# Kernel tuning notes

Hardware: AMD Instinct MI355X
Metric: run time of the kernel (lower is better)

The kernel has to match this reference:

```python
import jax, jax.numpy as jnp
import numpy as np

D_IN = 784
D_Z = 100
N_SAMP = 10
LOG_2PI = float(np.log(2.0 * np.pi))


def setup_inputs() -> dict:
    key = jax.random.key(0)
    ks = jax.random.split(key, 8)
    B = 16384
    x = jax.random.uniform(ks[0], (B, D_IN), dtype=jnp.float32)
    s = 0.05  # small init scale so softplus/sigmoid stay in a sane range
    W0 = jax.random.normal(ks[1], (D_Z, D_IN), dtype=jnp.float32) * s
    b0 = jax.random.normal(ks[2], (D_Z,), dtype=jnp.float32) * s
    W1 = jax.random.normal(ks[3], (D_Z, D_IN), dtype=jnp.float32) * s
    b1 = jax.random.normal(ks[4], (D_Z,), dtype=jnp.float32) * s
    W2 = jax.random.normal(ks[5], (D_IN, D_Z), dtype=jnp.float32) * s
    b2 = jax.random.normal(ks[6], (D_IN,), dtype=jnp.float32) * s
    eps = jax.random.normal(ks[7], (N_SAMP, D_Z), dtype=jnp.float32)  # pz.sample([10])
    return {"x": x, "W0": W0, "b0": b0, "W1": W1, "b1": b1, "W2": W2, "b2": b2, "eps": eps}


def reference(x, W0, b0, W1, b1, W2, b2, eps):
    # encoder: per-dim mean over the batch of softplus(Linear(x))
    mean = jnp.mean(jax.nn.softplus(x @ W0.T + b0), axis=0)        # [D_Z]
    cov = jnp.mean(jax.nn.softplus(x @ W1.T + b1), axis=0)         # [D_Z] (diag variances)
    # z = mean + covariance * eps, eps ~ N(0, I)
    z = mean + cov * eps                                           # [N_SAMP, D_Z]
    y = z @ W2.T + b2                                              # [N_SAMP, D_IN]
    p = jax.nn.sigmoid((2.0 * x[:, None, :] - 1.0) * y[None, :, :])  # [B, N_SAMP, D_IN]
    pv_z = jnp.prod(p, axis=-1) + 0.001                            # [B, N_SAMP]
    E_px_v = jnp.mean(jnp.log(pv_z))
    # diagonal-Gaussian log probs (equivalent to the MVN with eye*cov)
    log_pz = -0.5 * jnp.sum(z * z, axis=-1) - 0.5 * D_Z * LOG_2PI
    log_q = (-0.5 * jnp.sum((z - mean) ** 2 / cov, axis=-1)
             - 0.5 * jnp.sum(jnp.log(cov)) - 0.5 * D_Z * LOG_2PI)
    Dkl = jnp.mean(log_pz - log_q)
    return -(E_px_v + Dkl)
```

## Files before the change

kernel.cpp:

```cpp
#include <hip/hip_runtime.h>
#include <hip/hip_bf16.h>
#include <math.h>

#define NROWS 16384
#define DIN   784
#define DZ    100
#define NS    10
#define NCT   16
#define KTILES 25
#define BND_THR 45.0f
#define KTPAD 520

typedef unsigned short ushort_t;
typedef short bf16x8 __attribute__((ext_vector_type(8)));
typedef float f32x4  __attribute__((ext_vector_type(4)));

#define WS_Y2 208
#define WB_OFF_BYTES (64u * 1024u)

__device__ __forceinline__ float softplus_fast(float v) {
    float t = v * 1.44269504088896f;
    return (fmaxf(t, 0.f)
            + __builtin_amdgcn_logf(1.f + __builtin_amdgcn_exp2f(-fabsf(t))))
           * 0.69314718055995f;
}
__device__ __forceinline__ unsigned pack2(float lo, float hi) {
    float2 f2; f2.x = lo; f2.y = hi;
    __hip_bfloat162 h2 = __float22bfloat162_rn(f2);
    return *reinterpret_cast<unsigned*>(&h2);
}

__global__ __launch_bounds__(256) void wb_kernel(
    const float* __restrict__ W0, const float* __restrict__ W1,
    ushort_t* __restrict__ Wb, float* __restrict__ ws)
{
    if (blockIdx.x == 0) ws[threadIdx.x] = 0.f;
    int t = blockIdx.x * 256 + threadIdx.x;
    if (t >= KTILES * NCT * 64) return;
    int kt = t >> 10;
    int r  = t & 1023;
    int ct = r >> 6, l = r & 63;
    int col = ct * 16 + (l & 15);
    int k0  = kt * 32 + (l >> 4) * 8;
    uint4 o = make_uint4(0u, 0u, 0u, 0u);
    if (col < 200 && k0 < DIN) {
        const float* src = (col < 100 ? W0 + (size_t)col * DIN
                                      : W1 + (size_t)(col - 100) * DIN) + k0;
        float4 a = *(const float4*)src;
        float4 b = *(const float4*)(src + 4);
        o.x = pack2(a.x, a.y); o.y = pack2(a.z, a.w);
        o.z = pack2(b.x, b.y); o.w = pack2(b.z, b.w);
    }
    *(uint4*)(Wb + (size_t)t * 8) = o;
}

__global__ __launch_bounds__(1024) void colmean_g(
    const float* __restrict__ x, const ushort_t* __restrict__ Wb,
    const float* __restrict__ b0, const float* __restrict__ b1,
    float* __restrict__ ws)
{
    __shared__ ushort_t xls[4 * KTILES * KTPAD];
    __shared__ float red2[12][4][16];
    const int tid = threadIdx.x;
    const int lane = tid & 63, w = tid >> 6;
    const int row0 = blockIdx.x * 64;

    for (int slot = tid; slot < 6400; slot += 1024) {
        int r  = slot / 100;
        int sl = slot - r * 100;
        int kt = sl >> 2, kc = sl & 3;
        int k0 = kt * 32 + kc * 8;
        uint4 o = make_uint4(0u, 0u, 0u, 0u);
        if (k0 + 8 <= DIN) {
            const float* src = x + (size_t)(row0 + r) * DIN + k0;
            float4 a = *(const float4*)src, b = *(const float4*)(src + 4);
            o.x = pack2(a.x, a.y); o.y = pack2(a.z, a.w);
            o.z = pack2(b.x, b.y); o.w = pack2(b.z, b.w);
        }
        int l = (kc << 4) | (r & 15);
        *(uint4*)&xls[((size_t)(r >> 4) * KTILES + kt) * KTPAD + l * 8] = o;
    }
    __syncthreads();

    const int rt = w >> 2, ct0 = (w & 3) * 4;
    const ushort_t* ap  = xls + (size_t)rt * KTILES * KTPAD + lane * 8;
    const ushort_t* wbp = Wb + (size_t)ct0 * 512 + lane * 8;

    f32x4 acc[4];
#pragma unroll
    for (int jj = 0; jj < 4; ++jj) acc[jj] = (f32x4){0.f, 0.f, 0.f, 0.f};

    bf16x8 Aa, Ab;
    uint4  Ba[4], Bb[4];

    auto ld = [&](int kt, bf16x8& A, uint4 (&B)[4]) {
        A = *(const bf16x8*)(ap + (size_t)kt * KTPAD);
#pragma unroll
        for (int jj = 0; jj < 4; ++jj)
            B[jj] = *(const uint4*)(wbp + (size_t)kt * 8192 + jj * 512);
    };
    auto cp = [&](const bf16x8& A, const uint4 (&B)[4]) {
#pragma unroll
        for (int jj = 0; jj < 4; ++jj)
            acc[jj] = __builtin_amdgcn_mfma_f32_16x16x32_bf16(
                A, *(const bf16x8*)&B[jj], acc[jj], 0, 0, 0);
    };

    ld(0, Aa, Ba);
    for (int i = 0; i < 12; ++i) {
        ld(2 * i + 1, Ab, Bb);
        cp(Aa, Ba);
        ld(2 * i + 2, Aa, Ba);
        cp(Ab, Bb);
    }
    cp(Aa, Ba);

    float vj[4];
#pragma unroll
    for (int jj = 0; jj < 4; ++jj) {
        int j = (ct0 + jj) * 16 + (lane & 15);
        float bias = (j < 100) ? b0[j] : ((j < 200) ? b1[j - 100] : 0.f);
        float v = 0.f;
#pragma unroll
        for (int r = 0; r < 4; ++r) v += softplus_fast(acc[jj][r] + bias);
        v += __shfl_xor(v, 16);
        v += __shfl_xor(v, 32);
        vj[jj] = v;
    }
    if (rt > 0 && (lane >> 4) == 0) {
#pragma unroll
        for (int jj = 0; jj < 4; ++jj)
            red2[(rt - 1) * 4 + (w & 3)][jj][lane & 15] = vj[jj];
    }
    __syncthreads();
    if (rt == 0 && (lane >> 4) == 0) {
#pragma unroll
        for (int jj = 0; jj < 4; ++jj) {
            int j = (ct0 + jj) * 16 + (lane & 15);
            float v = vj[jj]
                    + red2[0 + (w & 3)][jj][lane & 15]
                    + red2[4 + (w & 3)][jj][lane & 15]
                    + red2[8 + (w & 3)][jj][lane & 15];
            if (j < 200) atomicAdd(&ws[j], v);
        }
    }
}

__global__ __launch_bounds__(256) void y2z_kernel(
    const float* __restrict__ W2, const float* __restrict__ b2,
    const float* __restrict__ eps, float* __restrict__ ws)
{
    int wid  = (int)((blockIdx.x * 256 + threadIdx.x) >> 6);
    int lane = threadIdx.x & 63;
    if (wid >= NS * DIN) return;
    int s = wid / DIN, i = wid % DIN;
    const float inv = 1.f / (float)NROWS;
    const float* wr = W2 + (size_t)i * DZ;
    const float* er = eps + (size_t)s * DZ;
    float p = 0.f;
    for (int d = lane; d < DZ; d += 64) {
        float zd = inv * (ws[d] + ws[100 + d] * er[d]);
        p += zd * wr[d];
    }
#pragma unroll
    for (int off = 32; off > 0; off >>= 1) p += __shfl_xor(p, off);
    if (lane == 0) ws[WS_Y2 + wid] = (p + b2[i]) * 1.4426950408889634f;
}

__global__ __launch_bounds__(256, 4) void pv_final_kernel(
    const float* __restrict__ x, float* __restrict__ ws,
    const float* __restrict__ eps, float* __restrict__ out, int nblocks)
{
    __shared__ ushort_t yf[KTILES * 512];
    __shared__ ushort_t ya[KTILES * 512];
    __shared__ float bsum;
    __shared__ int lastflag;
    __shared__ float dred[256];
    const int tid = threadIdx.x;
    const int lane = tid & 63, w = tid >> 6;

    for (int idx = tid; idx < KTILES * 64; idx += 256) {
        int kt = idx >> 6, l = idx & 63;
        int ss = l & 15, k0 = kt * 32 + (l >> 4) * 8;
        uint4 o = make_uint4(0u, 0u, 0u, 0u), oa = o;
        if (ss < NS && k0 < DIN) {
            const float* src = ws + WS_Y2 + ss * DIN + k0;
            float4 a = *(const float4*)src, b = *(const float4*)(src + 4);
            o.x = pack2(a.x, a.y); o.y = pack2(a.z, a.w);
            o.z = pack2(b.x, b.y); o.w = pack2(b.z, b.w);
            oa.x = o.x & 0x7FFF7FFFu; oa.y = o.y & 0x7FFF7FFFu;
            oa.z = o.z & 0x7FFF7FFFu; oa.w = o.w & 0x7FFF7FFFu;
        }
        *(uint4*)(yf + (size_t)idx * 8) = o;
        *(uint4*)(ya + (size_t)idx * 8) = oa;
    }
    if (tid == 0) { bsum = 0.f; lastflag = 0; }
    __syncthreads();

    const int tile = blockIdx.x * 4 + w;
    const int row  = tile * 16 + (lane & 15);
    const int kc   = lane >> 4;
    const int s    = lane & 15;
    const float* xp = x + (size_t)row * DIN;
    const float L001 = -6.90775527898f;

    f32x4 acc0 = (f32x4){0.f, 0.f, 0.f, 0.f};
    f32x4 acc1 = (f32x4){0.f, 0.f, 0.f, 0.f};
    float4 a0A, a1A, a0B, a1B;

    auto loadA = [&](int kt, float4& a0, float4& a1) {
        int k0 = kt * 32 + kc * 8;
        if (k0 + 8 > DIN) k0 = 768;
        a0 = *(const float4*)(xp + k0);
        a1 = *(const float4*)(xp + k0 + 4);
    };
    auto comp = [&](int kt, const float4& a0, const float4& a1) {
        bf16x8 nf; unsigned* p = (unsigned*)&nf;
        p[0] = pack2(1.f - 2.f * a0.x, 1.f - 2.f * a0.y);
        p[1] = pack2(1.f - 2.f * a0.z, 1.f - 2.f * a0.w);
        p[2] = pack2(1.f - 2.f * a1.x, 1.f - 2.f * a1.y);
        p[3] = pack2(1.f - 2.f * a1.z, 1.f - 2.f * a1.w);
        bf16x8 na; unsigned* q = (unsigned*)&na;
        q[0] = p[0] & 0x7FFF7FFFu; q[1] = p[1] & 0x7FFF7FFFu;
        q[2] = p[2] & 0x7FFF7FFFu; q[3] = p[3] & 0x7FFF7FFFu;
        bf16x8 fy = *(const bf16x8*)(yf + (size_t)kt * 512 + lane * 8);
        bf16x8 fa = *(const bf16x8*)(ya + (size_t)kt * 512 + lane * 8);
        acc0 = __builtin_amdgcn_mfma_f32_16x16x32_bf16(nf, fy, acc0, 0, 0, 0);
        acc1 = __builtin_amdgcn_mfma_f32_16x16x32_bf16(na, fa, acc1, 0, 0, 0);
    };

    loadA(0, a0A, a1A);
    for (int i = 0; i < 12; ++i) {
        loadA(2 * i + 1, a0B, a1B);
        comp(2 * i, a0A, a1A);
        loadA(2 * i + 2, a0A, a1A);
        comp(2 * i + 1, a0B, a1B);
    }
    comp(24, a0A, a1A);

    float bnd[4];
#pragma unroll
    for (int r = 0; r < 4; ++r) bnd[r] = 0.5f * (acc0[r] + acc1[r]);

    float wsum;
    bool lslow = (s < NS) &&
        (fminf(fminf(bnd[0], bnd[1]), fminf(bnd[2], bnd[3])) < BND_THR);
    unsigned long long m = __ballot(lslow);
    if (m == 0ull) {
        wsum = 160.f * L001;
    } else {
        int nslow = 0;
        float slowsum = 0.f;
#pragma unroll
        for (int r = 0; r < 4; ++r) {
            unsigned long long mr = __ballot((s < NS) && (bnd[r] < BND_THR));
            nslow += (int)__popcll(mr);
            while (mr) {
                int src = (int)__ffsll(mr) - 1; mr &= (mr - 1);
                int ss = src & 15;
                int rrow = tile * 16 + (src >> 4) * 4 + r;
                const float* xq = x + (size_t)rrow * DIN;
                const float* yq = ws + WS_Y2 + ss * DIN;
                float a = 0.f;
                for (int i = lane; i < DIN; i += 64)
                    a -= __builtin_amdgcn_logf(
                        1.f + __builtin_amdgcn_exp2f((1.f - 2.f * xq[i]) * yq[i]));
#pragma unroll
                for (int off = 32; off > 0; off >>= 1) a += __shfl_xor(a, off);
                slowsum += __logf(__builtin_amdgcn_exp2f(a) + 0.001f);
            }
        }
        wsum = (float)(160 - nslow) * L001 + slowsum;
    }
    if (lane == 0) atomicAdd(&bsum, wsum);
    __syncthreads();

    if (tid == 0) {
        atomicAdd(&ws[200], bsum);
        __threadfence();
        unsigned old = atomicAdd((unsigned*)&ws[202], 1u);
        if (old == (unsigned)(nblocks - 1)) lastflag = 1;
    }
    __syncthreads();
    if (lastflag) {
        __threadfence();
        float contrib = 0.f;
        if (tid < DZ) {
            const float inv = 1.f / (float)NROWS;
            float mm = ws[tid] * inv;
            float cc = ws[100 + tid] * inv;
            contrib = 0.5f * __logf(cc);
#pragma unroll
            for (int ss2 = 0; ss2 < NS; ++ss2) {
                float e = eps[ss2 * DZ + tid];
                float zz = mm + cc * e;
                contrib += (0.5f * cc * e * e - 0.5f * zz * zz) * (1.f / NS);
            }
        }
        dred[tid] = contrib;
        __syncthreads();
        for (int off = 128; off > 0; off >>= 1) {
            if (tid < off) dred[tid] += dred[tid + off];
            __syncthreads();
        }
        if (tid == 0) {
            float S = atomicAdd(&ws[200], 0.f);
            float E = S * (1.f / ((float)NROWS * (float)NS));
            out[0] = -(E + dred[0]);
        }
    }
}

extern "C" void kernel_launch(void* const* d_in, const int* in_sizes, int n_in,
                              void* d_out, int out_size, void* d_ws, size_t ws_size,
                              hipStream_t stream)
{
    const float* x   = (const float*)d_in[0];
    const float* W0  = (const float*)d_in[1];
    const float* b0  = (const float*)d_in[2];
    const float* W1  = (const float*)d_in[3];
    const float* b1  = (const float*)d_in[4];
    const float* W2  = (const float*)d_in[5];
    const float* b2  = (const float*)d_in[6];
    const float* eps = (const float*)d_in[7];
    float* out = (float*)d_out;
    float* ws  = (float*)d_ws;
    ushort_t* Wb = (ushort_t*)((char*)d_ws + WB_OFF_BYTES);

    wb_kernel<<<(KTILES * NCT * 64 + 255) / 256, 256, 0, stream>>>(W0, W1, Wb, ws);
    colmean_g<<<NROWS / 64, 1024, 0, stream>>>(x, Wb, b0, b1, ws);
    y2z_kernel<<<(NS * DIN * 64) / 256, 256, 0, stream>>>(W2, b2, eps, ws);
    pv_final_kernel<<<256, 256, 0, stream>>>(x, ws, eps, out, 256);
}
```

Measured before the change: 57.76 us.

## Fuse encoder, decoder and likelihood into one cooperative kernel with grid barrier

Merges the column-mean GEMM, the z/y decoder computation and the per-row likelihood pass into a single cooperative kernel that uses a global atomic barrier. The bf16 x tile held in LDS is reused for the second pass instead of re-reading x from global memory, and each block recomputes y in shared memory. The aim is to cut launch overhead and the second read of x. In exchange every block redundantly computes the 784x100x10 decoder product, and the kernel relies on co-residency of 256 blocks with about 150KB of LDS each. If the cooperative launch fails it falls back to the old three kernels.

```diff
diff --git a/kernel.cpp b/kernel.cpp
--- a/kernel.cpp
+++ b/kernel.cpp
@@ -10,6 +10,7 @@
 #define KTILES 25
 #define BND_THR 45.0f
 #define KTPAD 520
+#define NBLK  256
 
 typedef unsigned short ushort_t;
 typedef short bf16x8 __attribute__((ext_vector_type(8)));
@@ -17,6 +18,14 @@
 
 #define WS_Y2 208
 #define WB_OFF_BYTES (64u * 1024u)
+
+#define XLS_OFF   0
+#define YF_OFF    104000
+#define MCOV_OFF  129600
+#define ZL_OFF    130400
+#define RED_OFF   134400
+#define FLAGS_OFF 150784
+#define SMEM_SZ   150800
 
 __device__ __forceinline__ float softplus_fast(float v) {
     float t = v * 1.44269504088896f;
@@ -54,16 +63,25 @@
     *(uint4*)(Wb + (size_t)t * 8) = o;
 }
 
-__global__ __launch_bounds__(1024) void colmean_g(
+__global__ __launch_bounds__(1024) void fused_kernel(
     const float* __restrict__ x, const ushort_t* __restrict__ Wb,
     const float* __restrict__ b0, const float* __restrict__ b1,
-    float* __restrict__ ws)
+    const float* __restrict__ W2, const float* __restrict__ b2,
+    const float* __restrict__ eps, float* __restrict__ ws,
+    float* __restrict__ out)
 {
-    __shared__ ushort_t xls[4 * KTILES * KTPAD];
-    __shared__ float red2[12][4][16];
+    __shared__ __align__(16) unsigned char smem[SMEM_SZ];
+    ushort_t* xls  = (ushort_t*)(smem + XLS_OFF);
+    ushort_t* yfp  = (ushort_t*)(smem + YF_OFF);
+    float*    mcov = (float*)(smem + MCOV_OFF);
+    float*    zl   = (float*)(smem + ZL_OFF);
+    float*    redp = (float*)(smem + RED_OFF);
+    int*      flags= (int*)(smem + FLAGS_OFF);
+
     const int tid = threadIdx.x;
     const int lane = tid & 63, w = tid >> 6;
     const int row0 = blockIdx.x * 64;
+    if (tid == 0) flags[0] = 0;
 
     for (int slot = tid; slot < 6400; slot += 1024) {
         int r  = slot / 100;
@@ -82,6 +100,259 @@
     }
     __syncthreads();
 
+    {
+        const int rt = w >> 2, ct0 = (w & 3) * 4;
+        const ushort_t* ap  = xls + (size_t)rt * KTILES * KTPAD + lane * 8;
+        const ushort_t* wbp = Wb + (size_t)ct0 * 512 + lane * 8;
+
+        f32x4 acc[4];
+#pragma unroll
+        for (int jj = 0; jj < 4; ++jj) acc[jj] = (f32x4){0.f, 0.f, 0.f, 0.f};
+
+        bf16x8 Aa, Ab;
+        uint4  Ba[4], Bb[4];
+        auto ld = [&](int kt, bf16x8& A, uint4 (&B)[4]) {
+            A = *(const bf16x8*)(ap + (size_t)kt * KTPAD);
+#pragma unroll
+            for (int jj = 0; jj < 4; ++jj)
+                B[jj] = *(const uint4*)(wbp + (size_t)kt * 8192 + jj * 512);
+        };
+        auto cp = [&](const bf16x8& A, const uint4 (&B)[4]) {
+#pragma unroll
+            for (int jj = 0; jj < 4; ++jj)
+                acc[jj] = __builtin_amdgcn_mfma_f32_16x16x32_bf16(
+                    A, *(const bf16x8*)&B[jj], acc[jj], 0, 0, 0);
+        };
+        ld(0, Aa, Ba);
+        for (int i = 0; i < 12; ++i) {
+            ld(2 * i + 1, Ab, Bb);
+            cp(Aa, Ba);
+            ld(2 * i + 2, Aa, Ba);
+            cp(Ab, Bb);
+        }
+        cp(Aa, Ba);
+
+        float vj[4];
+#pragma unroll
+        for (int jj = 0; jj < 4; ++jj) {
+            int j = (ct0 + jj) * 16 + (lane & 15);
+            float bias = (j < 100) ? b0[j] : ((j < 200) ? b1[j - 100] : 0.f);
+            float v = 0.f;
+#pragma unroll
+            for (int r = 0; r < 4; ++r) v += softplus_fast(acc[jj][r] + bias);
+            v += __shfl_xor(v, 16);
+            v += __shfl_xor(v, 32);
+            vj[jj] = v;
+        }
+        if (rt > 0 && (lane >> 4) == 0) {
+#pragma unroll
+            for (int jj = 0; jj < 4; ++jj)
+                redp[(((rt - 1) * 4 + (w & 3)) * 4 + jj) * 16 + (lane & 15)] = vj[jj];
+        }
+        __syncthreads();
+        if (rt == 0 && (lane >> 4) == 0) {
+#pragma unroll
+            for (int jj = 0; jj < 4; ++jj) {
+                int j = (ct0 + jj) * 16 + (lane & 15);
+                float v = vj[jj]
+                        + redp[((0 + (w & 3)) * 4 + jj) * 16 + (lane & 15)]
+                        + redp[((4 + (w & 3)) * 4 + jj) * 16 + (lane & 15)]
+                        + redp[((8 + (w & 3)) * 4 + jj) * 16 + (lane & 15)];
+                if (j < 200) atomicAdd(&ws[j], v);
+            }
+        }
+        __syncthreads();
+    }
+
+    if (tid == 0) {
+        __threadfence();
+        atomicAdd((unsigned*)&ws[202], 1u);
+        while (__hip_atomic_load((unsigned*)&ws[202], __ATOMIC_RELAXED,
+                                 __HIP_MEMORY_SCOPE_AGENT) < (unsigned)NBLK) {
+            __builtin_amdgcn_s_sleep(2);
+        }
+    }
+    __syncthreads();
+
+    if (tid < 200)
+        mcov[tid] = __hip_atomic_load(&ws[tid], __ATOMIC_RELAXED,
+                                      __HIP_MEMORY_SCOPE_AGENT) * (1.f / (float)NROWS);
+    for (int i2 = tid; i2 < 1600; i2 += 1024)
+        ((uint4*)yfp)[i2] = make_uint4(0u, 0u, 0u, 0u);
+    __syncthreads();
+    if (tid < 1000) {
+        int s = tid / 100, d = tid - s * 100;
+        zl[tid] = mcov[d] + mcov[100 + d] * eps[s * DZ + d];
+    }
+    __syncthreads();
+    for (int i = tid; i < DIN; i += 1024) {
+        const float* wr = W2 + (size_t)i * DZ;
+        float p[NS];
+#pragma unroll
+        for (int s = 0; s < NS; ++s) p[s] = 0.f;
+        for (int d4 = 0; d4 < DZ; d4 += 4) {
+            float4 wv = *(const float4*)(wr + d4);
+#pragma unroll
+            for (int s = 0; s < NS; ++s) {
+                const float* zs = zl + s * DZ + d4;
+                p[s] += wv.x * zs[0] + wv.y * zs[1] + wv.z * zs[2] + wv.w * zs[3];
+            }
+        }
+        float bb = b2[i];
+        int kt = i >> 5, k = i & 31, ks2 = k >> 3, j = k & 7;
+#pragma unroll
+        for (int s = 0; s < NS; ++s) {
+            float v = (p[s] + bb) * 1.4426950408889634f;
+            __hip_bfloat16 h = __float2bfloat16(v);
+            yfp[((size_t)(kt * 64 + ks2 * 16 + s)) * 8 + j] = *(ushort_t*)&h;
+        }
+    }
+    __syncthreads();
+
+    {
+        const int rt = w >> 2, kseg = w & 3;
+        const ushort_t* ap = xls + (size_t)rt * KTILES * KTPAD + lane * 8;
+        f32x4 acc0 = (f32x4){0.f, 0.f, 0.f, 0.f};
+        f32x4 acc1 = (f32x4){0.f, 0.f, 0.f, 0.f};
+        for (int kt = kseg; kt < KTILES; kt += 4) {
+            uint4 X = *(const uint4*)(ap + (size_t)kt * KTPAD);
+            bf16x8 nf; unsigned* p = (unsigned*)&nf;
+            const unsigned* xw = (const unsigned*)&X;
+#pragma unroll
+            for (int i2 = 0; i2 < 4; ++i2) {
+                float lo = __uint_as_float(xw[i2] << 16);
+                float hi = __uint_as_float(xw[i2] & 0xFFFF0000u);
+                p[i2] = pack2(1.f - 2.f * lo, 1.f - 2.f * hi);
+            }
+            bf16x8 na; unsigned* q = (unsigned*)&na;
+            q[0] = p[0] & 0x7FFF7FFFu; q[1] = p[1] & 0x7FFF7FFFu;
+            q[2] = p[2] & 0x7FFF7FFFu; q[3] = p[3] & 0x7FFF7FFFu;
+            bf16x8 fy = *(const bf16x8*)(yfp + (size_t)kt * 512 + lane * 8);
+            bf16x8 fa; unsigned* fq = (unsigned*)&fa;
+            const unsigned* fp = (const unsigned*)&fy;
+            fq[0] = fp[0] & 0x7FFF7FFFu; fq[1] = fp[1] & 0x7FFF7FFFu;
+            fq[2] = fp[2] & 0x7FFF7FFFu; fq[3] = fp[3] & 0x7FFF7FFFu;
+            acc0 = __builtin_amdgcn_mfma_f32_16x16x32_bf16(nf, fy, acc0, 0, 0, 0);
+            acc1 = __builtin_amdgcn_mfma_f32_16x16x32_bf16(na, fa, acc1, 0, 0, 0);
+        }
+#pragma unroll
+        for (int r = 0; r < 4; ++r)
+            redp[((size_t)w * 64 + lane) * 4 + r] = 0.5f * (acc0[r] + acc1[r]);
+        __syncthreads();
+
+        if (kseg == 0) {
+            const int s = lane & 15;
+            const float L001 = -6.90775527898f;
+            float bnd[4];
+#pragma unroll
+            for (int r = 0; r < 4; ++r)
+                bnd[r] = redp[(((rt * 4 + 0) * 64) + lane) * 4 + r]
+                       + redp[(((rt * 4 + 1) * 64) + lane) * 4 + r]
+                       + redp[(((rt * 4 + 2) * 64) + lane) * 4 + r]
+                       + redp[(((rt * 4 + 3) * 64) + lane) * 4 + r];
+            float wsum;
+            bool lslow = (s < NS) &&
+                (fminf(fminf(bnd[0], bnd[1]), fminf(bnd[2], bnd[3])) < BND_THR);
+            unsigned long long m = __ballot(lslow);
+            if (m == 0ull) {
+                wsum = 160.f * L001;
+            } else {
+                int nslow = 0;
+                float slowsum = 0.f;
+#pragma unroll
+                for (int r = 0; r < 4; ++r) {
+                    unsigned long long mr = __ballot((s < NS) && (bnd[r] < BND_THR));
+                    nslow += (int)__popcll(mr);
+                    while (mr) {
+                        int src = (int)__ffsll(mr) - 1; mr &= (mr - 1);
+                        int ss = src & 15;
+                        int rrow = row0 + rt * 16 + (src >> 4) * 4 + r;
+                        const float* xq = x + (size_t)rrow * DIN;
+                        const float* zs = zl + ss * DZ;
+                        float a = 0.f;
+                        for (int i = lane; i < DIN; i += 64) {
+                            const float* wr = W2 + (size_t)i * DZ;
+                            float yi = 0.f;
+                            for (int d4 = 0; d4 < DZ; d4 += 4) {
+                                float4 wv = *(const float4*)(wr + d4);
+                                yi += wv.x * zs[d4] + wv.y * zs[d4 + 1]
+                                    + wv.z * zs[d4 + 2] + wv.w * zs[d4 + 3];
+                            }
+                            float y2i = (yi + b2[i]) * 1.4426950408889634f;
+                            a -= __builtin_amdgcn_logf(
+                                1.f + __builtin_amdgcn_exp2f((1.f - 2.f * xq[i]) * y2i));
+                        }
+#pragma unroll
+                        for (int off = 32; off > 0; off >>= 1) a += __shfl_xor(a, off);
+                        slowsum += __logf(__builtin_amdgcn_exp2f(a) + 0.001f);
+                    }
+                }
+                wsum = (float)(160 - nslow) * L001 + slowsum;
+            }
+            if (lane == 0) atomicAdd(&ws[200], wsum);
+        }
+        __syncthreads();
+    }
+
+    if (tid == 0) {
+        unsigned old = atomicAdd((unsigned*)&ws[203], 1u);
+        flags[0] = (old == (unsigned)(NBLK - 1)) ? 1 : 0;
+    }
+    __syncthreads();
+    if (flags[0]) {
+        float contrib = 0.f;
+        if (tid < DZ) {
+            float mm = mcov[tid], cc = mcov[100 + tid];
+            contrib = 0.5f * __logf(cc);
+#pragma unroll
+            for (int s = 0; s < NS; ++s) {
+                float e = eps[s * DZ + tid];
+                float zz = mm + cc * e;
+                contrib += (0.5f * cc * e * e - 0.5f * zz * zz) * (1.f / NS);
+            }
+        }
+        redp[tid] = contrib;
+        __syncthreads();
+        for (int off = 512; off > 0; off >>= 1) {
+            if (tid < off) redp[tid] += redp[tid + off];
+            __syncthreads();
+        }
+        if (tid == 0) {
+            float S = __hip_atomic_load(&ws[200], __ATOMIC_RELAXED,
+                                        __HIP_MEMORY_SCOPE_AGENT);
+            out[0] = -(S * (1.f / ((float)NROWS * (float)NS)) + redp[0]);
+        }
+    }
+}
+
+__global__ __launch_bounds__(1024) void colmean_g(
+    const float* __restrict__ x, const ushort_t* __restrict__ Wb,
+    const float* __restrict__ b0, const float* __restrict__ b1,
+    float* __restrict__ ws)
+{
+    __shared__ ushort_t xls[4 * KTILES * KTPAD];
+    __shared__ float red2[12][4][16];
+    const int tid = threadIdx.x;
+    const int lane = tid & 63, w = tid >> 6;
+    const int row0 = blockIdx.x * 64;
+
+    for (int slot = tid; slot < 6400; slot += 1024) {
+        int r  = slot / 100;
+        int sl = slot - r * 100;
+        int kt = sl >> 2, kc = sl & 3;
+        int k0 = kt * 32 + kc * 8;
+        uint4 o = make_uint4(0u, 0u, 0u, 0u);
+        if (k0 + 8 <= DIN) {
+            const float* src = x + (size_t)(row0 + r) * DIN + k0;
+            float4 a = *(const float4*)src, b = *(const float4*)(src + 4);
+            o.x = pack2(a.x, a.y); o.y = pack2(a.z, a.w);
+            o.z = pack2(b.x, b.y); o.w = pack2(b.z, b.w);
+        }
+        int l = (kc << 4) | (r & 15);
+        *(uint4*)&xls[((size_t)(r >> 4) * KTILES + kt) * KTPAD + l * 8] = o;
+    }
+    __syncthreads();
+
     const int rt = w >> 2, ct0 = (w & 3) * 4;
     const ushort_t* ap  = xls + (size_t)rt * KTILES * KTPAD + lane * 8;
     const ushort_t* wbp = Wb + (size_t)ct0 * 512 + lane * 8;
@@ -89,10 +360,8 @@
     f32x4 acc[4];
 #pragma unroll
     for (int jj = 0; jj < 4; ++jj) acc[jj] = (f32x4){0.f, 0.f, 0.f, 0.f};
-
     bf16x8 Aa, Ab;
     uint4  Ba[4], Bb[4];
-
     auto ld = [&](int kt, bf16x8& A, uint4 (&B)[4]) {
         A = *(const bf16x8*)(ap + (size_t)kt * KTPAD);
 #pragma unroll
@@ -105,7 +374,6 @@
             acc[jj] = __builtin_amdgcn_mfma_f32_16x16x32_bf16(
                 A, *(const bf16x8*)&B[jj], acc[jj], 0, 0, 0);
     };
-
     ld(0, Aa, Ba);
     for (int i = 0; i < 12; ++i) {
         ld(2 * i + 1, Ab, Bb);
@@ -228,7 +496,6 @@
         acc0 = __builtin_amdgcn_mfma_f32_16x16x32_bf16(nf, fy, acc0, 0, 0, 0);
         acc1 = __builtin_amdgcn_mfma_f32_16x16x32_bf16(na, fa, acc1, 0, 0, 0);
     };
-
     loadA(0, a0A, a1A);
     for (int i = 0; i < 12; ++i) {
         loadA(2 * i + 1, a0B, a1B);
@@ -241,7 +508,6 @@
     float bnd[4];
 #pragma unroll
     for (int r = 0; r < 4; ++r) bnd[r] = 0.5f * (acc0[r] + acc1[r]);
-
     float wsum;
     bool lslow = (s < NS) &&
         (fminf(fminf(bnd[0], bnd[1]), fminf(bnd[2], bnd[3])) < BND_THR);
@@ -278,7 +544,7 @@
     if (tid == 0) {
         atomicAdd(&ws[200], bsum);
         __threadfence();
-        unsigned old = atomicAdd((unsigned*)&ws[202], 1u);
+        unsigned old = atomicAdd((unsigned*)&ws[203], 1u);
         if (old == (unsigned)(nblocks - 1)) lastflag = 1;
     }
     __syncthreads();
@@ -328,7 +594,16 @@
     ushort_t* Wb = (ushort_t*)((char*)d_ws + WB_OFF_BYTES);
 
     wb_kernel<<<(KTILES * NCT * 64 + 255) / 256, 256, 0, stream>>>(W0, W1, Wb, ws);
-    colmean_g<<<NROWS / 64, 1024, 0, stream>>>(x, Wb, b0, b1, ws);
-    y2z_kernel<<<(NS * DIN * 64) / 256, 256, 0, stream>>>(W2, b2, eps, ws);
-    pv_final_kernel<<<256, 256, 0, stream>>>(x, ws, eps, out, 256);
-}
+
+    void* args[] = { (void*)&x, (void*)&Wb, (void*)&b0, (void*)&b1,
+                     (void*)&W2, (void*)&b2, (void*)&eps, (void*)&ws, (void*)&out };
+    hipError_t e = hipLaunchCooperativeKernel((void*)fused_kernel,
+                                              dim3(NBLK), dim3(1024),
+                                              args, 0, stream);
+    if (e != hipSuccess) {
+        (void)hipGetLastError();
+        colmean_g<<<NROWS / 64, 1024, 0, stream>>>(x, Wb, b0, b1, ws);
+        y2z_kernel<<<(NS * DIN * 64) / 256, 256, 0, stream>>>(W2, b2, eps, ws);
+        pv_final_kernel<<<256, 256, 0, stream>>>(x, ws, eps, out, 256);
+    }
+}
```

Result: slower. 107.6 us (+86.3%).

## Give each wave one column tile across all row tiles in colmean

Applied to the files above, without the earlier changes.

The column-mean GEMM kernel now assigns each of its 16 waves a single 16-column tile and all four 16-row tiles. Before, each wave took one row tile and four column tiles. Each wave therefore reads one bf16 weight fragment from global memory per k-step instead of four, and reads four x fragments from LDS instead of one. Per-column results are now complete within a wave, which removes the shared-memory cross-wave reduction and its barrier. The completion counter in the final kernel also moves to a different workspace slot; this depends on that slot being zeroed.

```diff
diff --git a/kernel.cpp b/kernel.cpp
--- a/kernel.cpp
+++ b/kernel.cpp
@@ -54,13 +54,12 @@
     *(uint4*)(Wb + (size_t)t * 8) = o;
 }
 
-__global__ __launch_bounds__(1024) void colmean_g(
+__global__ __launch_bounds__(1024) void colmean_h(
     const float* __restrict__ x, const ushort_t* __restrict__ Wb,
     const float* __restrict__ b0, const float* __restrict__ b1,
     float* __restrict__ ws)
 {
     __shared__ ushort_t xls[4 * KTILES * KTPAD];
-    __shared__ float red2[12][4][16];
     const int tid = threadIdx.x;
     const int lane = tid & 63, w = tid >> 6;
     const int row0 = blockIdx.x * 64;
@@ -82,28 +81,26 @@
     }
     __syncthreads();
 
-    const int rt = w >> 2, ct0 = (w & 3) * 4;
-    const ushort_t* ap  = xls + (size_t)rt * KTILES * KTPAD + lane * 8;
-    const ushort_t* wbp = Wb + (size_t)ct0 * 512 + lane * 8;
-
-    f32x4 acc[4];
-#pragma unroll
-    for (int jj = 0; jj < 4; ++jj) acc[jj] = (f32x4){0.f, 0.f, 0.f, 0.f};
-
-    bf16x8 Aa, Ab;
-    uint4  Ba[4], Bb[4];
-
-    auto ld = [&](int kt, bf16x8& A, uint4 (&B)[4]) {
-        A = *(const bf16x8*)(ap + (size_t)kt * KTPAD);
-#pragma unroll
-        for (int jj = 0; jj < 4; ++jj)
-            B[jj] = *(const uint4*)(wbp + (size_t)kt * 8192 + jj * 512);
+    const ushort_t* ap  = xls + lane * 8;
+    const ushort_t* wbp = Wb + (size_t)w * 512 + lane * 8;
+
+    f32x4 acc0 = (f32x4){0.f,0.f,0.f,0.f}, acc1 = acc0, acc2 = acc0, acc3 = acc0;
+
+    bf16x8 Aa[4], Ab[4];
+    uint4  Ba, Bb;
+
+    auto ld = [&](int kt, bf16x8 (&A)[4], uint4& B) {
+#pragma unroll
+        for (int rt = 0; rt < 4; ++rt)
+            A[rt] = *(const bf16x8*)(ap + (size_t)rt * KTILES * KTPAD + (size_t)kt * KTPAD);
+        B = *(const uint4*)(wbp + (size_t)kt * 8192);
     };
-    auto cp = [&](const bf16x8& A, const uint4 (&B)[4]) {
-#pragma unroll
-        for (int jj = 0; jj < 4; ++jj)
-            acc[jj] = __builtin_amdgcn_mfma_f32_16x16x32_bf16(
-                A, *(const bf16x8*)&B[jj], acc[jj], 0, 0, 0);
+    auto cp = [&](const bf16x8 (&A)[4], const uint4& B) {
+        bf16x8 bf = *(const bf16x8*)&B;
+        acc0 = __builtin_amdgcn_mfma_f32_16x16x32_bf16(A[0], bf, acc0, 0, 0, 0);
+        acc1 = __builtin_amdgcn_mfma_f32_16x16x32_bf16(A[1], bf, acc1, 0, 0, 0);
+        acc2 = __builtin_amdgcn_mfma_f32_16x16x32_bf16(A[2], bf, acc2, 0, 0, 0);
+        acc3 = __builtin_amdgcn_mfma_f32_16x16x32_bf16(A[3], bf, acc3, 0, 0, 0);
     };
 
     ld(0, Aa, Ba);
@@ -115,35 +112,16 @@
     }
     cp(Aa, Ba);
 
-    float vj[4];
-#pragma unroll
-    for (int jj = 0; jj < 4; ++jj) {
-        int j = (ct0 + jj) * 16 + (lane & 15);
-        float bias = (j < 100) ? b0[j] : ((j < 200) ? b1[j - 100] : 0.f);
-        float v = 0.f;
-#pragma unroll
-        for (int r = 0; r < 4; ++r) v += softplus_fast(acc[jj][r] + bias);
-        v += __shfl_xor(v, 16);
-        v += __shfl_xor(v, 32);
-        vj[jj] = v;
-    }
-    if (rt > 0 && (lane >> 4) == 0) {
-#pragma unroll
-        for (int jj = 0; jj < 4; ++jj)
-            red2[(rt - 1) * 4 + (w & 3)][jj][lane & 15] = vj[jj];
-    }
-    __syncthreads();
-    if (rt == 0 && (lane >> 4) == 0) {
-#pragma unroll
-        for (int jj = 0; jj < 4; ++jj) {
-            int j = (ct0 + jj) * 16 + (lane & 15);
-            float v = vj[jj]
-                    + red2[0 + (w & 3)][jj][lane & 15]
-                    + red2[4 + (w & 3)][jj][lane & 15]
-                    + red2[8 + (w & 3)][jj][lane & 15];
-            if (j < 200) atomicAdd(&ws[j], v);
-        }
-    }
+    const int j = w * 16 + (lane & 15);
+    const float bias = (j < 100) ? b0[j] : ((j < 200) ? b1[j - 100] : 0.f);
+    float v = 0.f;
+#pragma unroll
+    for (int r = 0; r < 4; ++r)
+        v += softplus_fast(acc0[r] + bias) + softplus_fast(acc1[r] + bias)
+           + softplus_fast(acc2[r] + bias) + softplus_fast(acc3[r] + bias);
+    v += __shfl_xor(v, 16);
+    v += __shfl_xor(v, 32);
+    if ((lane >> 4) == 0 && j < 200) atomicAdd(&ws[j], v);
 }
 
 __global__ __launch_bounds__(256) void y2z_kernel(
@@ -228,7 +206,6 @@
         acc0 = __builtin_amdgcn_mfma_f32_16x16x32_bf16(nf, fy, acc0, 0, 0, 0);
         acc1 = __builtin_amdgcn_mfma_f32_16x16x32_bf16(na, fa, acc1, 0, 0, 0);
     };
-
     loadA(0, a0A, a1A);
     for (int i = 0; i < 12; ++i) {
         loadA(2 * i + 1, a0B, a1B);
@@ -241,7 +218,6 @@
     float bnd[4];
 #pragma unroll
     for (int r = 0; r < 4; ++r) bnd[r] = 0.5f * (acc0[r] + acc1[r]);
-
     float wsum;
     bool lslow = (s < NS) &&
         (fminf(fminf(bnd[0], bnd[1]), fminf(bnd[2], bnd[3])) < BND_THR);
@@ -278,7 +254,7 @@
     if (tid == 0) {
         atomicAdd(&ws[200], bsum);
         __threadfence();
-        unsigned old = atomicAdd((unsigned*)&ws[202], 1u);
+        unsigned old = atomicAdd((unsigned*)&ws[203], 1u);
         if (old == (unsigned)(nblocks - 1)) lastflag = 1;
     }
     __syncthreads();
@@ -328,7 +304,7 @@
     ushort_t* Wb = (ushort_t*)((char*)d_ws + WB_OFF_BYTES);
 
     wb_kernel<<<(KTILES * NCT * 64 + 255) / 256, 256, 0, stream>>>(W0, W1, Wb, ws);
-    colmean_g<<<NROWS / 64, 1024, 0, stream>>>(x, Wb, b0, b1, ws);
+    colmean_h<<<NROWS / 64, 1024, 0, stream>>>(x, Wb, b0, b1, ws);
     y2z_kernel<<<(NS * DIN * 64) / 256, 256, 0, stream>>>(W2, b2, eps, ws);
     pv_final_kernel<<<256, 256, 0, stream>>>(x, ws, eps, out, 256);
 }
```

Result: faster. 50.86 us (median of 2 runs) (-11.9%).
